# Performance work log

Hardware: AMD Instinct MI355X
Metric: run time of the kernel (lower is better)

The kernel has to match this reference:

```python
import jax, jax.numpy as jnp
import numpy as np
import math

B, S, H = 2, 4096, 512
NUM_HEADS = 8
HEAD_DIM = H // NUM_HEADS
RECENCY_DECAY = 0.9


def setup_inputs() -> dict:
    key = jax.random.key(0)
    k1, k2, k3 = jax.random.split(key, 3)
    scale = 1.0 / math.sqrt(H)
    x = jax.random.normal(k1, (B, S, H), dtype=jnp.float32)
    w_qkv = jax.random.normal(k2, (3 * H, H), dtype=jnp.float32) * scale
    w_out = jax.random.normal(k3, (H, H), dtype=jnp.float32) * scale
    b_out = jnp.zeros((H,), dtype=jnp.float32)
    return {"x": x, "w_qkv": w_qkv, "w_out": w_out, "b_out": b_out}


def reference(x, w_qkv, w_out, b_out):
    batch, seq_len, hidden = x.shape
    nh, hd = NUM_HEADS, HEAD_DIM
    # qkv projection (no bias): torch Linear computes x @ W.T
    qkv = jnp.einsum('bsh,oh->bso', x, w_qkv)
    qkv = qkv.reshape(batch, seq_len, 3, nh, hd)
    q, k, v = jnp.transpose(qkv, (2, 0, 3, 1, 4))  # each [B, nh, S, hd]
    attn = jnp.einsum('bhqd,bhkd->bhqk', q, k) / math.sqrt(hd)
    # recency bias: positions[i, j] = j - i; bias = (j-i)*log(decay) for j<=i else 0
    pos = jnp.arange(seq_len)[None, :] - jnp.arange(seq_len)[:, None]
    bias = jnp.where(pos <= 0, pos.astype(jnp.float32) * math.log(RECENCY_DECAY),
                     jnp.zeros((), dtype=jnp.float32))
    attn = jax.nn.softmax(attn + bias[None, None, :, :], axis=-1)
    out = jnp.einsum('bhqk,bhkd->bqhd', attn, v).reshape(batch, seq_len, hidden)
    return jnp.einsum('bsh,oh->bso', out, w_out) + b_out
```

## Files before the change

### kernel.cpp

```cpp
#include <hip/hip_runtime.h>
#include <hip/hip_bf16.h>
#include <hip/hip_fp16.h>
#include <stdint.h>

#define B_   2
#define S_   4096
#define H_   512
#define NH_  8
#define HD_  64
#define M_   (B_*S_)
#define LOG2D (-0.15200309344504997f)
#define SC2   (0.18033688011112042f)

#define NFULL        4
#define NCHUNK       8

typedef __attribute__((ext_vector_type(8))) short bf16x8_t;
typedef __attribute__((ext_vector_type(4))) float f32x4_t;
typedef __attribute__((ext_vector_type(8))) _Float16 f16x8_t;

__device__ __forceinline__ void gl_lds16(const __hip_bfloat16* g, __hip_bfloat16* l) {
  __builtin_amdgcn_global_load_lds(
      (__attribute__((address_space(1))) void*)(g),
      (__attribute__((address_space(3))) void*)(l),
      16, 0, 0);
}

__device__ __forceinline__ bf16x8_t cvt8(float4 a, float4 b) {
  bf16x8_t r; __hip_bfloat16 h;
  h = __float2bfloat16(a.x); r[0] = *(short*)&h;
  h = __float2bfloat16(a.y); r[1] = *(short*)&h;
  h = __float2bfloat16(a.z); r[2] = *(short*)&h;
  h = __float2bfloat16(a.w); r[3] = *(short*)&h;
  h = __float2bfloat16(b.x); r[4] = *(short*)&h;
  h = __float2bfloat16(b.y); r[5] = *(short*)&h;
  h = __float2bfloat16(b.z); r[6] = *(short*)&h;
  h = __float2bfloat16(b.w); r[7] = *(short*)&h;
  return r;
}

__global__ __launch_bounds__(256)
void gemm_qkv(const float* __restrict__ A,
              const float* __restrict__ Bw,
              __hip_bfloat16* __restrict__ qb,
              __hip_bfloat16* __restrict__ kb,
              __hip_bfloat16* __restrict__ vtb) {
  __shared__ alignas(16) __hip_bfloat16 sA[128*64];
  __shared__ alignas(16) __hip_bfloat16 sB[128*64];
  const int tid  = threadIdx.x;
  const int wave = tid >> 6, lane = tid & 63;
  const int quad = lane >> 4, l15 = lane & 15;
  const int wr = (wave >> 1) * 64, wc = (wave & 1) * 64;

  const int nbx  = gridDim.x;
  const int flat = blockIdx.y * nbx + blockIdx.x;
  const int xcd  = flat & 7, sq = flat >> 3;
  const int rows_per_xcd = gridDim.y >> 3;
  const int by = xcd * rows_per_xcd + sq / nbx;
  const int bx = sq % nbx;
  const int m0 = by * 128, n0 = bx * 128;

  const int sub  = lane >> 3;
  const int plog = (lane & 7) ^ sub;

  f32x4_t acc[4][4] = {};

  for (int kt = 0; kt < H_; kt += 64) {
    __syncthreads();
    #pragma unroll
    for (int cc = 0; cc < 4; cc++) {
      int c   = wave * 4 + cc;
      int row = c * 8 + sub;
      const float* ga = A  + (size_t)(m0 + row) * H_ + kt + plog * 8;
      const float* gb = Bw + (size_t)(n0 + row) * H_ + kt + plog * 8;
      float4 a0 = *(const float4*)ga;
      float4 a1 = *(const float4*)(ga + 4);
      float4 b0 = *(const float4*)gb;
      float4 b1 = *(const float4*)(gb + 4);
      *(bf16x8_t*)(sA + c * 512 + lane * 8) = cvt8(a0, a1);
      *(bf16x8_t*)(sB + c * 512 + lane * 8) = cvt8(b0, b1);
    }
    __syncthreads();
    #pragma unroll
    for (int kh = 0; kh < 2; kh++) {
      bf16x8_t af[4], bfr[4];
      #pragma unroll
      for (int x = 0; x < 4; x++) {
        int row = wr + x * 16 + l15;
        int pos = kh * 4 + quad;
        af[x] = *(const bf16x8_t*)(sA + row * 64 + ((pos ^ (row & 7)) << 3));
      }
      #pragma unroll
      for (int y = 0; y < 4; y++) {
        int row = wc + y * 16 + l15;
        int pos = kh * 4 + quad;
        bfr[y] = *(const bf16x8_t*)(sB + row * 64 + ((pos ^ (row & 7)) << 3));
      }
      #pragma unroll
      for (int x = 0; x < 4; x++)
        #pragma unroll
        for (int y = 0; y < 4; y++)
          acc[x][y] = __builtin_amdgcn_mfma_f32_16x16x32_bf16(af[x], bfr[y], acc[x][y], 0, 0, 0);
    }
  }

  if ((n0 >> 9) == 2) {
    #pragma unroll
    for (int x = 0; x < 4; x++) {
      int gr = m0 + wr + x * 16 + quad * 4;
      int bb = gr >> 12, sb = gr & 4095;
      #pragma unroll
      for (int y = 0; y < 4; y++) {
        int rem = (n0 - 1024) + wc + y * 16 + l15;
        int h = rem >> 6, d = rem & 63;
        ushort4 o; __hip_bfloat16 hv;
        hv = __float2bfloat16(acc[x][y][0]); o.x = *(unsigned short*)&hv;
        hv = __float2bfloat16(acc[x][y][1]); o.y = *(unsigned short*)&hv;
        hv = __float2bfloat16(acc[x][y][2]); o.z = *(unsigned short*)&hv;
        hv = __float2bfloat16(acc[x][y][3]); o.w = *(unsigned short*)&hv;
        *(ushort4*)(vtb + ((size_t)(bb * NH_ + h) * HD_ + d) * S_ + sb) = o;
      }
    }
  } else {
    #pragma unroll
    for (int x = 0; x < 4; x++) {
      #pragma unroll
      for (int y = 0; y < 4; y++) {
        #pragma unroll
        for (int r = 0; r < 4; r++) {
          int gr = m0 + wr + x*16 + quad*4 + r;
          int gc = n0 + wc + y*16 + l15;
          float v = acc[x][y][r];
          int bb = gr >> 12, s = gr & 4095;
          int t  = gc >> 9,  rem = gc & 511;
          int h  = rem >> 6, d = rem & 63;
          __hip_bfloat16 hv = __float2bfloat16(v);
          int bh = bb * NH_ + h;
          if (t == 0) qb[((size_t)bh * S_ + s) * HD_ + d] = hv;
          else        kb[((size_t)bh * S_ + s) * HD_ + d] = hv;
        }
      }
    }
  }
}

__device__ __forceinline__ void stage_kv(const __hip_bfloat16* __restrict__ kb,
                                         const __hip_bfloat16* __restrict__ vtb,
                                         int bh, int j0,
                                         __hip_bfloat16* dK, __hip_bfloat16* dV,
                                         int wave, int lane, int sub, int plog) {
  if (wave < 2) {
    #pragma unroll
    for (int cc = 0; cc < 4; cc++) {
      int c = wave * 4 + cc;
      gl_lds16(kb + ((size_t)bh * S_ + j0 + c * 8 + sub) * HD_ + plog * 8, dK + c * 512);
    }
  } else {
    #pragma unroll
    for (int cc = 0; cc < 4; cc++) {
      int c = (wave - 2) * 4 + cc;
      gl_lds16(vtb + ((size_t)bh * HD_ + c * 8 + sub) * S_ + j0 + plog * 8, dV + c * 512);
    }
  }
}

__global__ __launch_bounds__(256)
void attn_kernel(const __hip_bfloat16* __restrict__ qb,
                 const __hip_bfloat16* __restrict__ kb,
                 const __hip_bfloat16* __restrict__ vtb,
                 __hip_bfloat16* __restrict__ ob,
                 __half* __restrict__ pO,
                 float* __restrict__ pl) {
  __shared__ alignas(16) __hip_bfloat16 sK[2][64*64];
  __shared__ alignas(16) __hip_bfloat16 sV[2][64*64];
  __shared__ alignas(16) __hip_bfloat16 sP[4][16*64];

  const int tid  = threadIdx.x;
  const int wave = tid >> 6, lane = tid & 63;
  const int quad = lane >> 4, l15 = lane & 15;
  const int w  = blockIdx.x;
  const int bh = blockIdx.y;

  int q0, jt0, niter, chunk = 0;
  bool direct;
  if (w < 60) { q0 = 256 + w * 64; jt0 = 0; niter = 4; direct = true; }
  else { int t = w - 60; chunk = t & 7; q0 = (t >> 3) * 64; jt0 = chunk * 8; niter = 8; direct = false; }

  const __hip_bfloat16* qrow = qb + ((size_t)bh * S_ + q0 + wave * 16 + l15) * HD_;
  bf16x8_t aQ0 = *(const bf16x8_t*)(qrow + quad * 8);
  bf16x8_t aQ1 = *(const bf16x8_t*)(qrow + 32 + quad * 8);

  f32x4_t accO[4] = {};
  float l_r[4], negM2[4];
  const int row_i = q0 + wave * 16 + quad * 4;
  #pragma unroll
  for (int r = 0; r < 4; r++) {
    l_r[r] = 0.f;
    negM2[r] = -(17.312340f - LOG2D * (float)(row_i + r));
  }

  const int sub  = lane >> 3;
  const int plog = (lane & 7) ^ sub;
  __hip_bfloat16* sPw = &sP[wave][0];

  stage_kv(kb, vtb, bh, jt0 * 64, &sK[0][0], &sV[0][0], wave, lane, sub, plog);

  for (int it = 0; it < niter; ++it) {
    const int cur = it & 1;
    __syncthreads();
    if (it < niter - 1)
      stage_kv(kb, vtb, bh, (jt0 + it + 1) * 64,
               &sK[1 - cur][0], &sV[1 - cur][0], wave, lane, sub, plog);
    const __hip_bfloat16* cK = &sK[cur][0];
    const __hip_bfloat16* cV = &sV[cur][0];
    const int j0 = (jt0 + it) * 64;

    f32x4_t sfr[4];
    #pragma unroll
    for (int ni = 0; ni < 4; ni++) {
      int row = ni * 16 + l15;
      f32x4_t a = {};
      bf16x8_t b0 = *(const bf16x8_t*)(cK + row * 64 + ((quad       ^ (row & 7)) << 3));
      bf16x8_t b1 = *(const bf16x8_t*)(cK + row * 64 + (((quad + 4) ^ (row & 7)) << 3));
      a = __builtin_amdgcn_mfma_f32_16x16x32_bf16(aQ0, b0, a, 0, 0, 0);
      a = __builtin_amdgcn_mfma_f32_16x16x32_bf16(aQ1, b1, a, 0, 0, 0);
      sfr[ni] = a;
    }

    #pragma unroll
    for (int r = 0; r < 4; r++) {
      const float d0 = (float)(j0 + l15 - (row_i + r));
      const int row = quad * 4 + r;
      float psum = 0.f;
      #pragma unroll
      for (int ni = 0; ni < 4; ni++) {
        float dij = d0 + (float)(ni * 16);
        float arg = fmaf(fminf(dij, 0.f), LOG2D, fmaf(sfr[ni][r], SC2, negM2[r]));
        float p = __builtin_amdgcn_exp2f(arg);
        psum += p;
        int col = ni * 16 + l15;
        sPw[row * 64 + (((col >> 3) ^ (row & 7)) << 3) + (col & 7)] = __float2bfloat16(p);
      }
      l_r[r] += psum;
    }
    __builtin_amdgcn_sched_barrier(0);
    __builtin_amdgcn_s_waitcnt(0xC07F);
    __builtin_amdgcn_sched_barrier(0);

    bf16x8_t aP0 = *(const bf16x8_t*)(sPw + l15 * 64 + ((quad       ^ (l15 & 7)) << 3));
    bf16x8_t aP1 = *(const bf16x8_t*)(sPw + l15 * 64 + (((quad + 4) ^ (l15 & 7)) << 3));
    #pragma unroll
    for (int nd = 0; nd < 4; nd++) {
      int row = nd * 16 + l15;
      bf16x8_t b0 = *(const bf16x8_t*)(cV + row * 64 + ((quad       ^ (row & 7)) << 3));
      bf16x8_t b1 = *(const bf16x8_t*)(cV + row * 64 + (((quad + 4) ^ (row & 7)) << 3));
      accO[nd] = __builtin_amdgcn_mfma_f32_16x16x32_bf16(aP0, b0, accO[nd], 0, 0, 0);
      accO[nd] = __builtin_amdgcn_mfma_f32_16x16x32_bf16(aP1, b1, accO[nd], 0, 0, 0);
    }
    __builtin_amdgcn_sched_barrier(0);
  }

  #pragma unroll
  for (int r = 0; r < 4; r++) {
    float l = l_r[r];
    #pragma unroll
    for (int msk = 1; msk < 16; msk <<= 1) l += __shfl_xor(l, msk, 64);
    l_r[r] = l;
  }

  if (direct) {
    const int b = bh >> 3, h = bh & 7;
    #pragma unroll
    for (int r = 0; r < 4; r++) {
      float invr = 1.0f / l_r[r];
      #pragma unroll
      for (int nd = 0; nd < 4; nd++) {
        int srow = q0 + wave * 16 + quad * 4 + r;
        int col  = h * HD_ + nd * 16 + l15;
        ob[((size_t)b * S_ + srow) * H_ + col] = __float2bfloat16(accO[nd][r] * invr);
      }
    }
  } else {
    const int qt = q0 >> 6;
    size_t base = ((size_t)bh * NFULL + qt) * NCHUNK + chunk;
    __half* po = pO + base * 4096;
    #pragma unroll
    for (int nd = 0; nd < 4; nd++)
      #pragma unroll
      for (int r = 0; r < 4; r++)
        po[(wave*16 + quad*4 + r) * 64 + nd*16 + l15] = __float2half(accO[nd][r]);
    if (l15 == 0) {
      #pragma unroll
      for (int r = 0; r < 4; r++)
        pl[base * 64 + wave*16 + quad*4 + r] = l_r[r];
    }
  }
}

__global__ __launch_bounds__(256)
void gemm_out(const __hip_bfloat16* __restrict__ ab,
              const float* __restrict__ Bw,
              const __half* __restrict__ pO,
              const float* __restrict__ pl,
              float* __restrict__ outp,
              const float* __restrict__ bias) {
  __shared__ alignas(16) __hip_bfloat16 sA[128*64];
  __shared__ alignas(16) __hip_bfloat16 sB[128*64];
  const int tid  = threadIdx.x;
  const int wave = tid >> 6, lane = tid & 63;
  const int quad = lane >> 4, l15 = lane & 15;
  const int wr = (wave >> 1) * 64, wc = (wave & 1) * 64;

  const int nbx  = gridDim.x;
  const int flat = blockIdx.y * nbx + blockIdx.x;
  const int xcd  = flat & 7, sq = flat >> 3;
  const int rows_per_xcd = gridDim.y >> 3;
  const int by = xcd * rows_per_xcd + sq / nbx;
  const int bx = sq % nbx;
  const int m0 = by * 128, n0 = bx * 128;
  const bool comb = (by & 31) < 2;

  const int sub  = lane >> 3;
  const int plog = (lane & 7) ^ sub;

  f32x4_t acc[4][4] = {};

  for (int kt = 0; kt < H_; kt += 64) {
    __syncthreads();
    if (comb) {
      const int h  = kt >> 6;
      const int bb = m0 >> 12;
      const int bh = bb * NH_ + h;
      #pragma unroll
      for (int cc = 0; cc < 4; cc++) {
        int c   = wave * 4 + cc;
        int row = c * 8 + sub;
        int s   = (m0 & 4095) + row;
        int qt  = s >> 6, rq = s & 63;
        size_t base0 = ((size_t)bh * NFULL + qt) * NCHUNK;
        float L = 0.f;
        float o[8] = {};
        #pragma unroll
        for (int ch = 0; ch < NCHUNK; ch++) {
          L += pl[(base0 + ch) * 64 + rq];
          f16x8_t v = *(const f16x8_t*)(pO + (base0 + ch) * 4096 + rq * 64 + plog * 8);
          #pragma unroll
          for (int k = 0; k < 8; k++) o[k] += (float)v[k];
        }
        float inv = 1.0f / L;
        bf16x8_t rr;
        #pragma unroll
        for (int k = 0; k < 8; k++) {
          __hip_bfloat16 hv = __float2bfloat16(o[k] * inv);
          rr[k] = *(short*)&hv;
        }
        *(bf16x8_t*)(sA + c * 512 + lane * 8) = rr;
      }
    } else {
      #pragma unroll
      for (int cc = 0; cc < 4; cc++) {
        int c   = wave * 4 + cc;
        int row = c * 8 + sub;
        gl_lds16(ab + (size_t)(m0 + row) * H_ + kt + plog * 8, sA + c * 512);
      }
    }
    #pragma unroll
    for (int cc = 0; cc < 4; cc++) {
      int c   = wave * 4 + cc;
      int row = c * 8 + sub;
      const float* gb = Bw + (size_t)(n0 + row) * H_ + kt + plog * 8;
      float4 b0 = *(const float4*)gb;
      float4 b1 = *(const float4*)(gb + 4);
      *(bf16x8_t*)(sB + c * 512 + lane * 8) = cvt8(b0, b1);
    }
    __syncthreads();
    #pragma unroll
    for (int kh = 0; kh < 2; kh++) {
      bf16x8_t af[4], bfr[4];
      #pragma unroll
      for (int x = 0; x < 4; x++) {
        int row = wr + x * 16 + l15;
        int pos = kh * 4 + quad;
        af[x] = *(const bf16x8_t*)(sA + row * 64 + ((pos ^ (row & 7)) << 3));
      }
      #pragma unroll
      for (int y = 0; y < 4; y++) {
        int row = wc + y * 16 + l15;
        int pos = kh * 4 + quad;
        bfr[y] = *(const bf16x8_t*)(sB + row * 64 + ((pos ^ (row & 7)) << 3));
      }
      #pragma unroll
      for (int x = 0; x < 4; x++)
        #pragma unroll
        for (int y = 0; y < 4; y++)
          acc[x][y] = __builtin_amdgcn_mfma_f32_16x16x32_bf16(af[x], bfr[y], acc[x][y], 0, 0, 0);
    }
  }

  #pragma unroll
  for (int x = 0; x < 4; x++) {
    #pragma unroll
    for (int y = 0; y < 4; y++) {
      #pragma unroll
      for (int r = 0; r < 4; r++) {
        int gr = m0 + wr + x*16 + quad*4 + r;
        int gc = n0 + wc + y*16 + l15;
        outp[(size_t)gr * H_ + gc] = acc[x][y][r] + bias[gc];
      }
    }
  }
}

extern "C" void kernel_launch(void* const* d_in, const int* in_sizes, int n_in,
                              void* d_out, int out_size, void* d_ws, size_t ws_size,
                              hipStream_t stream) {
  const float* x     = (const float*)d_in[0];
  const float* w_qkv = (const float*)d_in[1];
  const float* w_out = (const float*)d_in[2];
  const float* b_out = (const float*)d_in[3];
  float* out = (float*)d_out;

  char* ws = (char*)d_ws;
  __hip_bfloat16* ab  = (__hip_bfloat16*)(ws);
  __hip_bfloat16* qb  = (__hip_bfloat16*)(ws + (8u  << 20));
  __hip_bfloat16* kb  = (__hip_bfloat16*)(ws + (16u << 20));
  __hip_bfloat16* vtb = (__hip_bfloat16*)(ws + (24u << 20));
  __half*         pO  = (__half*)(ws + (32u << 20));
  float*          pl  = (float*)(ws + (36u << 20));

  gemm_qkv<<<dim3(12, 64), dim3(256), 0, stream>>>(x, w_qkv, qb, kb, vtb);
  attn_kernel<<<dim3(60 + NFULL * NCHUNK, B_ * NH_), dim3(256), 0, stream>>>(qb, kb, vtb, ab, pO, pl);
  gemm_out<<<dim3(4, 64), dim3(256), 0, stream>>>(ab, w_out, pO, pl, out, b_out);
}
```

Measured before the change: 164.4 us.

## Register-prefetch next K tile in both GEMMs and widen gemm_out to 512 threads

Both GEMM kernels now load the next 64-wide K slice of A and B from global memory into registers while the current slice is staged in LDS and consumed by MFMAs. This hides global load latency behind compute. Barriers become an explicit lgkmcnt wait plus s_barrier so outstanding global prefetches are not drained. gemm_out also doubles its threads to 512 with 8 waves each owning a 64x32 tile, raising per-block parallelism. The cost is more registers per thread, and the launch bounds request 3 and 2 blocks per CU respectively.

```diff
diff --git a/kernel.cpp b/kernel.cpp
--- a/kernel.cpp
+++ b/kernel.cpp
@@ -24,6 +24,11 @@
       (__attribute__((address_space(1))) void*)(g),
       (__attribute__((address_space(3))) void*)(l),
       16, 0, 0);
+}
+
+__device__ __forceinline__ void wg_barrier_lds() {
+  asm volatile("s_waitcnt lgkmcnt(0)" ::: "memory");
+  __builtin_amdgcn_s_barrier();
 }
 
 __device__ __forceinline__ bf16x8_t cvt8(float4 a, float4 b) {
@@ -39,7 +44,7 @@
   return r;
 }
 
-__global__ __launch_bounds__(256)
+__global__ __launch_bounds__(256, 3)
 void gemm_qkv(const float* __restrict__ A,
               const float* __restrict__ Bw,
               __hip_bfloat16* __restrict__ qb,
@@ -65,22 +70,36 @@
 
   f32x4_t acc[4][4] = {};
 
+  float4 pa0[4], pa1[4], pb0[4], pb1[4];
+  #pragma unroll
+  for (int cc = 0; cc < 4; cc++) {
+    int row = (wave * 4 + cc) * 8 + sub;
+    const float* ga = A  + (size_t)(m0 + row) * H_ + plog * 8;
+    const float* gb = Bw + (size_t)(n0 + row) * H_ + plog * 8;
+    pa0[cc] = *(const float4*)ga; pa1[cc] = *(const float4*)(ga + 4);
+    pb0[cc] = *(const float4*)gb; pb1[cc] = *(const float4*)(gb + 4);
+  }
+
   for (int kt = 0; kt < H_; kt += 64) {
-    __syncthreads();
+    wg_barrier_lds();
     #pragma unroll
     for (int cc = 0; cc < 4; cc++) {
-      int c   = wave * 4 + cc;
-      int row = c * 8 + sub;
-      const float* ga = A  + (size_t)(m0 + row) * H_ + kt + plog * 8;
-      const float* gb = Bw + (size_t)(n0 + row) * H_ + kt + plog * 8;
-      float4 a0 = *(const float4*)ga;
-      float4 a1 = *(const float4*)(ga + 4);
-      float4 b0 = *(const float4*)gb;
-      float4 b1 = *(const float4*)(gb + 4);
-      *(bf16x8_t*)(sA + c * 512 + lane * 8) = cvt8(a0, a1);
-      *(bf16x8_t*)(sB + c * 512 + lane * 8) = cvt8(b0, b1);
-    }
-    __syncthreads();
+      int c = wave * 4 + cc;
+      *(bf16x8_t*)(sA + c * 512 + lane * 8) = cvt8(pa0[cc], pa1[cc]);
+      *(bf16x8_t*)(sB + c * 512 + lane * 8) = cvt8(pb0[cc], pb1[cc]);
+    }
+    if (kt + 64 < H_) {
+      #pragma unroll
+      for (int cc = 0; cc < 4; cc++) {
+        int row = (wave * 4 + cc) * 8 + sub;
+        const float* ga = A  + (size_t)(m0 + row) * H_ + kt + 64 + plog * 8;
+        const float* gb = Bw + (size_t)(n0 + row) * H_ + kt + 64 + plog * 8;
+        pa0[cc] = *(const float4*)ga; pa1[cc] = *(const float4*)(ga + 4);
+        pb0[cc] = *(const float4*)gb; pb1[cc] = *(const float4*)(gb + 4);
+      }
+    }
+    wg_barrier_lds();
+    __builtin_amdgcn_sched_barrier(0);
     #pragma unroll
     for (int kh = 0; kh < 2; kh++) {
       bf16x8_t af[4], bfr[4];
@@ -297,7 +316,7 @@
   }
 }
 
-__global__ __launch_bounds__(256)
+__global__ __launch_bounds__(512, 2)
 void gemm_out(const __hip_bfloat16* __restrict__ ab,
               const float* __restrict__ Bw,
               const __half* __restrict__ pO,
@@ -309,7 +328,7 @@
   const int tid  = threadIdx.x;
   const int wave = tid >> 6, lane = tid & 63;
   const int quad = lane >> 4, l15 = lane & 15;
-  const int wr = (wave >> 1) * 64, wc = (wave & 1) * 64;
+  const int wr = (wave >> 2) * 64, wc = (wave & 3) * 32;
 
   const int nbx  = gridDim.x;
   const int flat = blockIdx.y * nbx + blockIdx.x;
@@ -323,17 +342,27 @@
   const int sub  = lane >> 3;
   const int plog = (lane & 7) ^ sub;
 
-  f32x4_t acc[4][4] = {};
+  f32x4_t acc[4][2] = {};
+
+  bf16x8_t prA[2]; float4 pb0[2], pb1[2];
+  #pragma unroll
+  for (int cc = 0; cc < 2; cc++) {
+    int row = (wave * 2 + cc) * 8 + sub;
+    if (!comb)
+      prA[cc] = *(const bf16x8_t*)(ab + (size_t)(m0 + row) * H_ + plog * 8);
+    const float* gb = Bw + (size_t)(n0 + row) * H_ + plog * 8;
+    pb0[cc] = *(const float4*)gb; pb1[cc] = *(const float4*)(gb + 4);
+  }
 
   for (int kt = 0; kt < H_; kt += 64) {
-    __syncthreads();
+    wg_barrier_lds();
     if (comb) {
       const int h  = kt >> 6;
       const int bb = m0 >> 12;
       const int bh = bb * NH_ + h;
       #pragma unroll
-      for (int cc = 0; cc < 4; cc++) {
-        int c   = wave * 4 + cc;
+      for (int cc = 0; cc < 2; cc++) {
+        int c   = wave * 2 + cc;
         int row = c * 8 + sub;
         int s   = (m0 & 4095) + row;
         int qt  = s >> 6, rq = s & 63;
@@ -358,25 +387,27 @@
       }
     } else {
       #pragma unroll
-      for (int cc = 0; cc < 4; cc++) {
-        int c   = wave * 4 + cc;
-        int row = c * 8 + sub;
-        gl_lds16(ab + (size_t)(m0 + row) * H_ + kt + plog * 8, sA + c * 512);
-      }
-    }
-    #pragma unroll
-    for (int cc = 0; cc < 4; cc++) {
-      int c   = wave * 4 + cc;
-      int row = c * 8 + sub;
-      const float* gb = Bw + (size_t)(n0 + row) * H_ + kt + plog * 8;
-      float4 b0 = *(const float4*)gb;
-      float4 b1 = *(const float4*)(gb + 4);
-      *(bf16x8_t*)(sB + c * 512 + lane * 8) = cvt8(b0, b1);
-    }
-    __syncthreads();
+      for (int cc = 0; cc < 2; cc++)
+        *(bf16x8_t*)(sA + (wave * 2 + cc) * 512 + lane * 8) = prA[cc];
+    }
+    #pragma unroll
+    for (int cc = 0; cc < 2; cc++)
+      *(bf16x8_t*)(sB + (wave * 2 + cc) * 512 + lane * 8) = cvt8(pb0[cc], pb1[cc]);
+    if (kt + 64 < H_) {
+      #pragma unroll
+      for (int cc = 0; cc < 2; cc++) {
+        int row = (wave * 2 + cc) * 8 + sub;
+        if (!comb)
+          prA[cc] = *(const bf16x8_t*)(ab + (size_t)(m0 + row) * H_ + kt + 64 + plog * 8);
+        const float* gb = Bw + (size_t)(n0 + row) * H_ + kt + 64 + plog * 8;
+        pb0[cc] = *(const float4*)gb; pb1[cc] = *(const float4*)(gb + 4);
+      }
+    }
+    wg_barrier_lds();
+    __builtin_amdgcn_sched_barrier(0);
     #pragma unroll
     for (int kh = 0; kh < 2; kh++) {
-      bf16x8_t af[4], bfr[4];
+      bf16x8_t af[4], bfr[2];
       #pragma unroll
       for (int x = 0; x < 4; x++) {
         int row = wr + x * 16 + l15;
@@ -384,7 +415,7 @@
         af[x] = *(const bf16x8_t*)(sA + row * 64 + ((pos ^ (row & 7)) << 3));
       }
       #pragma unroll
-      for (int y = 0; y < 4; y++) {
+      for (int y = 0; y < 2; y++) {
         int row = wc + y * 16 + l15;
         int pos = kh * 4 + quad;
         bfr[y] = *(const bf16x8_t*)(sB + row * 64 + ((pos ^ (row & 7)) << 3));
@@ -392,7 +423,7 @@
       #pragma unroll
       for (int x = 0; x < 4; x++)
         #pragma unroll
-        for (int y = 0; y < 4; y++)
+        for (int y = 0; y < 2; y++)
           acc[x][y] = __builtin_amdgcn_mfma_f32_16x16x32_bf16(af[x], bfr[y], acc[x][y], 0, 0, 0);
     }
   }
@@ -400,7 +431,7 @@
   #pragma unroll
   for (int x = 0; x < 4; x++) {
     #pragma unroll
-    for (int y = 0; y < 4; y++) {
+    for (int y = 0; y < 2; y++) {
       #pragma unroll
       for (int r = 0; r < 4; r++) {
         int gr = m0 + wr + x*16 + quad*4 + r;
@@ -430,5 +461,5 @@
 
   gemm_qkv<<<dim3(12, 64), dim3(256), 0, stream>>>(x, w_qkv, qb, kb, vtb);
   attn_kernel<<<dim3(60 + NFULL * NCHUNK, B_ * NH_), dim3(256), 0, stream>>>(qb, kb, vtb, ab, pO, pl);
-  gemm_out<<<dim3(4, 64), dim3(256), 0, stream>>>(ab, w_out, pO, pl, out, b_out);
-}
+  gemm_out<<<dim3(4, 64), dim3(512), 0, stream>>>(ab, w_out, pO, pl, out, b_out);
+}
```

Measured after the change: 168.7 us. +2.6%, slower.
